# Performance work log

Hardware: AMD Instinct MI355X
Metric: run time of the kernel (lower is better)

The kernel has to match this reference:

```python
import jax, jax.numpy as jnp
import numpy as np

EMBED_DIM = 1024
N_HEADS = 16
DK = EMBED_DIM // N_HEADS


def setup_inputs() -> dict:
    key = jax.random.key(0)
    ks = jax.random.split(key, 9)
    s = 1.0 / np.sqrt(EMBED_DIM)
    d = EMBED_DIM
    return {
        "x": jax.random.normal(ks[0], (2, 2048, d), dtype=jnp.float32),
        "Wq": jax.random.uniform(ks[1], (d, d), jnp.float32, -s, s),
        "bq": jax.random.uniform(ks[2], (d,), jnp.float32, -s, s),
        "Wk": jax.random.uniform(ks[3], (d, d), jnp.float32, -s, s),
        "bk": jax.random.uniform(ks[4], (d,), jnp.float32, -s, s),
        "Wv": jax.random.uniform(ks[5], (d, d), jnp.float32, -s, s),
        "bv": jax.random.uniform(ks[6], (d,), jnp.float32, -s, s),
        "Wo": jax.random.uniform(ks[7], (d, d), jnp.float32, -s, s),
        "bo": jax.random.uniform(ks[8], (d,), jnp.float32, -s, s),
    }


def reference(x, Wq, bq, Wk, bk, Wv, bv, Wo, bo):
    B, S, D = x.shape
    H, dk = N_HEADS, DK
    # QKV projections
    q = (x @ Wq + bq).reshape(B, S, H, dk).transpose(0, 2, 1, 3)  # [B,H,S,dk]
    k = (x @ Wk + bk).reshape(B, S, H, dk).transpose(0, 2, 1, 3)
    v = (x @ Wv + bv).reshape(B, S, H, dk).transpose(0, 2, 1, 3)
    # scaled dot-product attention with full score matrix (faithful to source)
    scores = jnp.einsum("bhqd,bhkd->bhqk", q, k) / jnp.sqrt(jnp.float32(dk))
    attn = jax.nn.softmax(scores, axis=-1)
    out = jnp.einsum("bhqk,bhkd->bhqd", attn, v)  # [B,H,S,dk]
    out = out.transpose(0, 2, 1, 3).reshape(B, S, D)
    return out @ Wo + bo
```

## Files before the change

### kernel.cpp

```cpp
#include <hip/hip_runtime.h>

typedef unsigned short u16;
typedef unsigned int u32;
typedef __attribute__((ext_vector_type(8))) short short8;
typedef __attribute__((ext_vector_type(4))) float float4v;

struct alignas(8) U16x4 { u16 x, y, z, w; };

__device__ __forceinline__ u16 f2b(float f) {
    union { float f; unsigned int u; } v; v.f = f;
    unsigned int r = (v.u >> 16) & 1u;
    v.u += 0x7fffu + r;
    return (u16)(v.u >> 16);
}

__device__ __forceinline__ float b2f(u16 u) {
    union { unsigned int u; float f; } v; v.u = ((u32)u) << 16; return v.f;
}

__device__ __forceinline__ void gld16(const u16* g, u16* l) {
    __builtin_amdgcn_global_load_lds(
        (const __attribute__((address_space(1))) void*)g,
        (__attribute__((address_space(3))) void*)l, 16, 0, 0);
}

__device__ __forceinline__ short8 frag8(const u16* base, int row, int cg) {
    return *(const short8*)(base + row * 64 + ((cg ^ (row & 7)) << 3));
}

__global__ __launch_bounds__(256) void prep_kernel(
    const float* __restrict__ x, const float* __restrict__ W0,
    const float* __restrict__ W1, const float* __restrict__ W2,
    const float* __restrict__ W3, u16* __restrict__ xb,
    u16* __restrict__ T0, u16* __restrict__ T1,
    u16* __restrict__ T2, u16* __restrict__ T3) {
    __shared__ float tile[32][33];
    int id = blockIdx.x;
    if (id < 4096) {
        size_t i = ((size_t)id * 256 + threadIdx.x) * 4;
        float4 v = *(const float4*)(x + i);
        U16x4 o;
        o.x = f2b(v.x); o.y = f2b(v.y); o.z = f2b(v.z); o.w = f2b(v.w);
        *(U16x4*)(xb + i) = o;
        return;
    }
    int r = id - 4096;
    int z = r >> 10, tl = r & 1023;
    const float* W = (z == 0) ? W0 : (z == 1) ? W1 : (z == 2) ? W2 : W3;
    u16* T = (z == 0) ? T0 : (z == 1) ? T1 : (z == 2) ? T2 : T3;
    int t = threadIdx.x;
    int tx = t & 31, ty = t >> 5;
    int bn = (tl & 31) * 32, bk = (tl >> 5) * 32;
#pragma unroll
    for (int p = 0; p < 4; ++p) {
        int k = ty + p * 8;
        tile[k][tx] = W[(size_t)(bk + k) * 1024 + bn + tx];
    }
    __syncthreads();
#pragma unroll
    for (int p = 0; p < 4; ++p) {
        int n = ty + p * 8;
        T[(size_t)(bn + n) * 1024 + bk + tx] = f2b(tile[tx][n]);
    }
}

__global__ __launch_bounds__(512, 2) void qkv_kernel(
    const u16* __restrict__ X,
    const u16* __restrict__ WqT, const u16* __restrict__ WkT, const u16* __restrict__ WvT,
    const float* __restrict__ bq, const float* __restrict__ bk, const float* __restrict__ bv,
    u16* __restrict__ Qo, u16* __restrict__ Ko, u16* __restrict__ VTo) {
    __shared__ __align__(16) u16 As[128 * 64];
    __shared__ __align__(16) u16 Bs[3][128 * 64];
    int id = blockIdx.x;
    int m = (id & 7) | (((id >> 3) & 3) << 3);
    int n = id >> 5;
    int t = threadIdx.x;
    int m0 = m * 128, n0 = n * 128;
    int lane = t & 63, wid = t >> 6;
    int wr = wid >> 2, wc = wid & 3;
    int l16 = lane & 15, quad = lane >> 4;
    int rl = lane >> 3, cs = lane & 7;

    int tileid = wid >> 1, half = wid & 1;
    const u16* gsrc = (tileid == 0) ? X : (tileid == 1) ? WqT
                     : (tileid == 2) ? WkT : WvT;
    int gbase = (tileid == 0) ? m0 : n0;
    u16* ldst = (tileid == 0) ? As : &Bs[tileid - 1][0];

    float4v acc[3][4][2];
    float4v zero4 = {0.f, 0.f, 0.f, 0.f};
#pragma unroll
    for (int z = 0; z < 3; ++z)
#pragma unroll
        for (int i = 0; i < 4; ++i)
#pragma unroll
            for (int j = 0; j < 2; ++j) acc[z][i][j] = zero4;

    for (int k0 = 0; k0 < 1024; k0 += 64) {
        __syncthreads();
#pragma unroll
        for (int p = 0; p < 8; ++p) {
            int q = half * 8 + p;
            int row = q * 8 + rl;
            int c = cs ^ (row & 7);
            gld16(gsrc + (size_t)(gbase + row) * 1024 + k0 + c * 8, ldst + q * 512);
        }
        __syncthreads();
#pragma unroll
        for (int ks = 0; ks < 64; ks += 32) {
            int cg = (ks >> 3) + quad;
            short8 af[4];
#pragma unroll
            for (int i = 0; i < 4; ++i)
                af[i] = frag8(As, wr * 64 + i * 16 + l16, cg);
#pragma unroll
            for (int z = 0; z < 3; ++z) {
                short8 bf[2];
#pragma unroll
                for (int j = 0; j < 2; ++j)
                    bf[j] = frag8(&Bs[z][0], wc * 32 + j * 16 + l16, cg);
#pragma unroll
                for (int i = 0; i < 4; ++i)
#pragma unroll
                    for (int j = 0; j < 2; ++j)
                        acc[z][i][j] = __builtin_amdgcn_mfma_f32_16x16x32_bf16(
                            af[i], bf[j], acc[z][i][j], 0, 0, 0);
            }
        }
    }

    const float QSCALE = 0.18033688011112042f;
#pragma unroll
    for (int j = 0; j < 2; ++j) {
        int n1 = n0 + wc * 32 + j * 16 + l16;
        float bql = bq[n1], bkl = bk[n1], bvl = bv[n1];
#pragma unroll
        for (int i = 0; i < 4; ++i) {
            int mbase = m0 + wr * 64 + i * 16 + quad * 4;
#pragma unroll
            for (int r = 0; r < 4; ++r) {
                Qo[(size_t)(mbase + r) * 1024 + n1] =
                    f2b((acc[0][i][j][r] + bql) * QSCALE);
                Ko[(size_t)(mbase + r) * 1024 + n1] =
                    f2b(acc[1][i][j][r] + bkl);
            }
            int bidx = mbase >> 11, s = mbase & 2047;
            size_t base =
                ((size_t)((bidx * 16 + (n1 >> 6)) * 64 + (n1 & 63))) * 2048 + s;
            U16x4 pk;
            pk.x = f2b(acc[2][i][j][0] + bvl);
            pk.y = f2b(acc[2][i][j][1] + bvl);
            pk.z = f2b(acc[2][i][j][2] + bvl);
            pk.w = f2b(acc[2][i][j][3] + bvl);
            *(U16x4*)(VTo + base) = pk;
        }
    }
}

__global__ __launch_bounds__(256) void oproj_kernel(const u16* __restrict__ X,
                                                    const u16* __restrict__ WoT,
                                                    const float* __restrict__ bias,
                                                    float* __restrict__ out) {
    __shared__ __align__(16) u16 As[64 * 64];
    __shared__ __align__(16) u16 Bs[128 * 64];
    int id = blockIdx.x;
    int m = (id & 7) | (((id >> 3) & 7) << 3);
    int n = id >> 6;
    int t = threadIdx.x;
    int m0 = m * 64, n0 = n * 128;
    int lane = t & 63, wid = t >> 6;
    int l16 = lane & 15, quad = lane >> 4;
    int rl = lane >> 3, cs = lane & 7;

    float4v acc[4][2];
    float4v zero4 = {0.f, 0.f, 0.f, 0.f};
#pragma unroll
    for (int i = 0; i < 4; ++i)
#pragma unroll
        for (int j = 0; j < 2; ++j) acc[i][j] = zero4;

    for (int k0 = 0; k0 < 1024; k0 += 64) {
        __syncthreads();
#pragma unroll
        for (int p = 0; p < 2; ++p) {
            int blk = wid * 2 + p;
            int row = blk * 8 + rl;
            int c = cs ^ (row & 7);
            gld16(X + (size_t)(m0 + row) * 1024 + k0 + c * 8, As + blk * 512);
        }
#pragma unroll
        for (int p = 0; p < 4; ++p) {
            int blk = wid * 4 + p;
            int row = blk * 8 + rl;
            int c = cs ^ (row & 7);
            gld16(WoT + (size_t)(n0 + row) * 1024 + k0 + c * 8, Bs + blk * 512);
        }
        __syncthreads();
#pragma unroll
        for (int ks = 0; ks < 64; ks += 32) {
            int cg = (ks >> 3) + quad;
            short8 af[4], bf[2];
#pragma unroll
            for (int i = 0; i < 4; ++i) af[i] = frag8(As, i * 16 + l16, cg);
#pragma unroll
            for (int j = 0; j < 2; ++j) bf[j] = frag8(Bs, wid * 32 + j * 16 + l16, cg);
#pragma unroll
            for (int i = 0; i < 4; ++i)
#pragma unroll
                for (int j = 0; j < 2; ++j)
                    acc[i][j] = __builtin_amdgcn_mfma_f32_16x16x32_bf16(
                        af[i], bf[j], acc[i][j], 0, 0, 0);
        }
    }

#pragma unroll
    for (int j = 0; j < 2; ++j) {
        int n1 = n0 + wid * 32 + j * 16 + l16;
        float bvl = bias[n1];
#pragma unroll
        for (int i = 0; i < 4; ++i) {
            int mbase = m0 + i * 16 + quad * 4;
#pragma unroll
            for (int r = 0; r < 4; ++r)
                out[(size_t)(mbase + r) * 1024 + n1] = acc[i][j][r] + bvl;
        }
    }
}

__global__ __launch_bounds__(256, 2) void flash_kernel(const u16* __restrict__ Q,
                                                       const u16* __restrict__ Kn,
                                                       const u16* __restrict__ VT,
                                                       u16* __restrict__ Opart,
                                                       float* __restrict__ lpart) {
    __shared__ __align__(16) u16 Ks[2][64 * 64];
    __shared__ __align__(16) u16 Vs[2][64 * 64];
    __shared__ __align__(16) u16 Ps[256 * 64];

    int id = blockIdx.x;
    int bh = (id & 7) | (((id >> 3) & 3) << 3);
    int rest = id >> 5;
    int qb = rest & 7, kvz = rest >> 3;
    int b = bh >> 4, h = bh & 15;
    int t = threadIdx.x;
    int wid = t >> 6, lane = t & 63;
    int l16 = lane & 15, quad = lane >> 4;
    int rl = lane >> 3, cs = lane & 7;
    int q0 = qb * 256 + wid * 64;
    size_t kbase = (size_t)(b * 2048) * 1024 + h * 64;
    size_t vbase = (size_t)(bh * 64) * 2048;
    int kv0 = kvz * 1024;

    short8 qf[4][2];
#pragma unroll
    for (int j = 0; j < 4; ++j)
#pragma unroll
        for (int kk = 0; kk < 2; ++kk)
            qf[j][kk] = *(const short8*)(
                Q + ((size_t)(b * 2048 + q0 + j * 16 + l16)) * 1024 + h * 64 +
                kk * 32 + quad * 8);

    float4v oacc[4][4];
    float lreg[4];
    float4v zero4 = {0.f, 0.f, 0.f, 0.f};
#pragma unroll
    for (int ip = 0; ip < 4; ++ip) {
        lreg[ip] = 0.f;
#pragma unroll
        for (int jd = 0; jd < 4; ++jd) oacc[ip][jd] = zero4;
    }

#define STAGE_KV(buf, kv)                                                     \
    {                                                                         \
        _Pragma("unroll") for (int p2 = 0; p2 < 2; ++p2) {                    \
            int p = wid * 2 + p2;                                             \
            int row = p * 8 + rl;                                             \
            int c = cs ^ (row & 7);                                           \
            gld16(Kn + kbase + (size_t)((kv) + row) * 1024 + c * 8,           \
                  &Ks[buf][p * 512]);                                         \
            gld16(VT + vbase + (size_t)row * 2048 + (kv) + c * 8,             \
                  &Vs[buf][p * 512]);                                         \
        }                                                                     \
    }

    STAGE_KV(0, kv0);

    for (int kvi = 0; kvi < 16; ++kvi) {
        int buf = kvi & 1;
        __syncthreads();
        if (kvi + 1 < 16) STAGE_KV(buf ^ 1, kv0 + (kvi + 1) * 64);

#pragma unroll
        for (int i = 0; i < 4; ++i) {
            float4v sacc[4];
#pragma unroll
            for (int j = 0; j < 4; ++j) sacc[j] = zero4;
            __builtin_amdgcn_s_setprio(1);
#pragma unroll
            for (int kk = 0; kk < 2; ++kk) {
                short8 kf = frag8(&Ks[buf][0], i * 16 + l16, kk * 4 + quad);
#pragma unroll
                for (int j = 0; j < 4; ++j)
                    sacc[j] = __builtin_amdgcn_mfma_f32_16x16x32_bf16(
                        kf, qf[j][kk], sacc[j], 0, 0, 0);
            }
            __builtin_amdgcn_s_setprio(0);
#pragma unroll
            for (int j = 0; j < 4; ++j) {
                float e0f = __builtin_amdgcn_exp2f(sacc[j][0]);
                float e1f = __builtin_amdgcn_exp2f(sacc[j][1]);
                float e2f = __builtin_amdgcn_exp2f(sacc[j][2]);
                float e3f = __builtin_amdgcn_exp2f(sacc[j][3]);
                lreg[j] += (e0f + e1f) + (e2f + e3f);
                u32 e0 = __float_as_uint(e0f) + 0x8000u;
                u32 e1 = __float_as_uint(e1f) + 0x8000u;
                u32 e2 = __float_as_uint(e2f) + 0x8000u;
                u32 e3 = __float_as_uint(e3f) + 0x8000u;
                uint2 pk;
                pk.x = __builtin_amdgcn_perm(e1, e0, 0x07060302u);
                pk.y = __builtin_amdgcn_perm(e3, e2, 0x07060302u);
                int prow = wid * 64 + j * 16 + l16;
                *(uint2*)(Ps + prow * 64 +
                          (((i * 2 + (quad >> 1)) ^ (prow & 7)) << 3) +
                          ((quad & 1) << 2)) = pk;
            }
        }

        __builtin_amdgcn_s_setprio(1);
#pragma unroll
        for (int kk = 0; kk < 2; ++kk) {
            int cg = kk * 4 + quad;
            short8 pf[4];
#pragma unroll
            for (int ip = 0; ip < 4; ++ip)
                pf[ip] = frag8(Ps, wid * 64 + ip * 16 + l16, cg);
#pragma unroll
            for (int jd = 0; jd < 4; ++jd) {
                short8 vf = frag8(&Vs[buf][0], jd * 16 + l16, cg);
#pragma unroll
                for (int ip = 0; ip < 4; ++ip)
                    oacc[ip][jd] = __builtin_amdgcn_mfma_f32_16x16x32_bf16(
                        pf[ip], vf, oacc[ip][jd], 0, 0, 0);
            }
        }
        __builtin_amdgcn_s_setprio(0);
    }
#undef STAGE_KV

#pragma unroll
    for (int j = 0; j < 4; ++j) {
        lreg[j] += __shfl_xor(lreg[j], 16);
        lreg[j] += __shfl_xor(lreg[j], 32);
    }

    size_t obase = (size_t)kvz * 4194304;
#pragma unroll
    for (int ip = 0; ip < 4; ++ip)
#pragma unroll
        for (int r = 0; r < 4; ++r) {
            int q = q0 + ip * 16 + quad * 4 + r;
#pragma unroll
            for (int jd = 0; jd < 4; ++jd)
                Opart[obase + ((size_t)(b * 2048 + q)) * 1024 + h * 64 +
                      jd * 16 + l16] = f2b(oacc[ip][jd][r]);
        }
    if (quad == 0) {
#pragma unroll
        for (int j = 0; j < 4; ++j) {
            int q = q0 + j * 16 + l16;
            lpart[kvz * 65536 + (b * 2048 + q) * 16 + h] = lreg[j];
        }
    }
}

__global__ __launch_bounds__(256) void combine_kernel(const u16* __restrict__ Op,
                                                      const float* __restrict__ lp,
                                                      u16* __restrict__ out) {
    int idx = blockIdx.x * 256 + threadIdx.x;
    size_t i = (size_t)idx * 4;
    int qg = idx >> 8;
    int d = (idx & 255) * 4;
    int h = d >> 6;
    float l0 = lp[qg * 16 + h], l1 = lp[65536 + qg * 16 + h];
    float inv = 1.0f / (l0 + l1);
    U16x4 o0 = *(const U16x4*)(Op + i);
    U16x4 o1 = *(const U16x4*)(Op + 4194304 + i);
    U16x4 o;
    o.x = f2b((b2f(o0.x) + b2f(o1.x)) * inv);
    o.y = f2b((b2f(o0.y) + b2f(o1.y)) * inv);
    o.z = f2b((b2f(o0.z) + b2f(o1.z)) * inv);
    o.w = f2b((b2f(o0.w) + b2f(o1.w)) * inv);
    *(U16x4*)(out + i) = o;
}

extern "C" void kernel_launch(void* const* d_in, const int* in_sizes, int n_in,
                              void* d_out, int out_size, void* d_ws, size_t ws_size,
                              hipStream_t stream) {
    const float* x  = (const float*)d_in[0];
    const float* Wq = (const float*)d_in[1];
    const float* bq = (const float*)d_in[2];
    const float* Wk = (const float*)d_in[3];
    const float* bk = (const float*)d_in[4];
    const float* Wv = (const float*)d_in[5];
    const float* bv = (const float*)d_in[6];
    const float* Wo = (const float*)d_in[7];
    const float* bo = (const float*)d_in[8];
    float* out = (float*)d_out;

    char* ws = (char*)d_ws;
    const size_t MB = 1024 * 1024;
    u16* xb  = (u16*)(ws);
    u16* wqt = (u16*)(ws + 8 * MB);
    u16* wkt = (u16*)(ws + 10 * MB);
    u16* wvt = (u16*)(ws + 12 * MB);
    u16* wot = (u16*)(ws + 14 * MB);
    u16* qb_ = (u16*)(ws + 16 * MB);
    u16* kb_ = (u16*)(ws + 24 * MB);
    u16* vt_ = (u16*)(ws + 32 * MB);
    u16* ab_ = (u16*)(ws + 40 * MB);
    u16* op_ = (u16*)(ws + 48 * MB);
    float* lp_ = (float*)(ws + 64 * MB);

    prep_kernel<<<8192, 256, 0, stream>>>(x, Wq, Wk, Wv, Wo, xb,
                                          wqt, wkt, wvt, wot);
    qkv_kernel<<<256, 512, 0, stream>>>(xb, wqt, wkt, wvt, bq, bk, bv,
                                        qb_, kb_, vt_);
    flash_kernel<<<512, 256, 0, stream>>>(qb_, kb_, vt_, op_, lp_);
    combine_kernel<<<4096, 256, 0, stream>>>(op_, lp_, ab_);
    oproj_kernel<<<512, 256, 0, stream>>>(ab_, wot, bo, out);
}
```

Measured before the change: 193.5 us.

## Keep softmax probabilities in registers via permuted K rows, drop LDS P buffer

The flash kernel no longer writes the exponentiated scores to shared memory and reads them back as MFMA A-operands. Instead, K rows are staged in a permuted order so that each lane's S accumulator fragment already matches the layout needed for the P·V MFMA, and packed bf16 probabilities are fed straight from registers. Dropping the 32KB P buffer and halving the queries per block (128 instead of 256, grid doubled) lowers LDS use and register pressure, allowing 4 blocks per CU. The cost is that K/V tiles are reloaded by twice as many blocks, and each wave does fewer MFMAs per K/V fragment load.

```diff
diff --git a/kernel.cpp b/kernel.cpp
--- a/kernel.cpp
+++ b/kernel.cpp
@@ -4,6 +4,7 @@
 typedef unsigned int u32;
 typedef __attribute__((ext_vector_type(8))) short short8;
 typedef __attribute__((ext_vector_type(4))) float float4v;
+typedef __attribute__((ext_vector_type(4))) unsigned int uint4v;
 
 struct alignas(8) U16x4 { u16 x, y, z, w; };
 
@@ -227,43 +228,42 @@
     }
 }
 
-__global__ __launch_bounds__(256, 2) void flash_kernel(const u16* __restrict__ Q,
+__global__ __launch_bounds__(256, 4) void flash_kernel(const u16* __restrict__ Q,
                                                        const u16* __restrict__ Kn,
                                                        const u16* __restrict__ VT,
                                                        u16* __restrict__ Opart,
                                                        float* __restrict__ lpart) {
     __shared__ __align__(16) u16 Ks[2][64 * 64];
     __shared__ __align__(16) u16 Vs[2][64 * 64];
-    __shared__ __align__(16) u16 Ps[256 * 64];
 
     int id = blockIdx.x;
     int bh = (id & 7) | (((id >> 3) & 3) << 3);
     int rest = id >> 5;
-    int qb = rest & 7, kvz = rest >> 3;
+    int qb = rest & 15, kvz = rest >> 4;
     int b = bh >> 4, h = bh & 15;
     int t = threadIdx.x;
     int wid = t >> 6, lane = t & 63;
     int l16 = lane & 15, quad = lane >> 4;
     int rl = lane >> 3, cs = lane & 7;
-    int q0 = qb * 256 + wid * 64;
+    int q0 = qb * 128 + wid * 32;
     size_t kbase = (size_t)(b * 2048) * 1024 + h * 64;
     size_t vbase = (size_t)(bh * 64) * 2048;
     int kv0 = kvz * 1024;
 
-    short8 qf[4][2];
-#pragma unroll
-    for (int j = 0; j < 4; ++j)
+    short8 qf[2][2];
+#pragma unroll
+    for (int j = 0; j < 2; ++j)
 #pragma unroll
         for (int kk = 0; kk < 2; ++kk)
             qf[j][kk] = *(const short8*)(
                 Q + ((size_t)(b * 2048 + q0 + j * 16 + l16)) * 1024 + h * 64 +
                 kk * 32 + quad * 8);
 
-    float4v oacc[4][4];
-    float lreg[4];
+    float4v oacc[2][4];
+    float lreg[2];
     float4v zero4 = {0.f, 0.f, 0.f, 0.f};
 #pragma unroll
-    for (int ip = 0; ip < 4; ++ip) {
+    for (int ip = 0; ip < 2; ++ip) {
         lreg[ip] = 0.f;
 #pragma unroll
         for (int jd = 0; jd < 4; ++jd) oacc[ip][jd] = zero4;
@@ -275,7 +275,9 @@
             int p = wid * 2 + p2;                                             \
             int row = p * 8 + rl;                                             \
             int c = cs ^ (row & 7);                                           \
-            gld16(Kn + kbase + (size_t)((kv) + row) * 1024 + c * 8,           \
+            int key = (((row >> 4) & 1) << 5) | (((row >> 2) & 3) << 3) |     \
+                      (((row >> 5) & 1) << 2) | (row & 3);                    \
+            gld16(Kn + kbase + (size_t)((kv) + key) * 1024 + c * 8,           \
                   &Ks[buf][p * 512]);                                         \
             gld16(VT + vbase + (size_t)row * 2048 + (kv) + c * 8,             \
                   &Vs[buf][p * 512]);                                         \
@@ -289,39 +291,32 @@
         __syncthreads();
         if (kvi + 1 < 16) STAGE_KV(buf ^ 1, kv0 + (kvi + 1) * 64);
 
+        u32 pw[2][4][2];
 #pragma unroll
         for (int i = 0; i < 4; ++i) {
-            float4v sacc[4];
-#pragma unroll
-            for (int j = 0; j < 4; ++j) sacc[j] = zero4;
+            float4v s0 = zero4, s1 = zero4;
             __builtin_amdgcn_s_setprio(1);
 #pragma unroll
             for (int kk = 0; kk < 2; ++kk) {
                 short8 kf = frag8(&Ks[buf][0], i * 16 + l16, kk * 4 + quad);
-#pragma unroll
-                for (int j = 0; j < 4; ++j)
-                    sacc[j] = __builtin_amdgcn_mfma_f32_16x16x32_bf16(
-                        kf, qf[j][kk], sacc[j], 0, 0, 0);
+                s0 = __builtin_amdgcn_mfma_f32_16x16x32_bf16(kf, qf[0][kk], s0, 0, 0, 0);
+                s1 = __builtin_amdgcn_mfma_f32_16x16x32_bf16(kf, qf[1][kk], s1, 0, 0, 0);
             }
             __builtin_amdgcn_s_setprio(0);
 #pragma unroll
-            for (int j = 0; j < 4; ++j) {
-                float e0f = __builtin_amdgcn_exp2f(sacc[j][0]);
-                float e1f = __builtin_amdgcn_exp2f(sacc[j][1]);
-                float e2f = __builtin_amdgcn_exp2f(sacc[j][2]);
-                float e3f = __builtin_amdgcn_exp2f(sacc[j][3]);
+            for (int j = 0; j < 2; ++j) {
+                float4v s = (j == 0) ? s0 : s1;
+                float e0f = __builtin_amdgcn_exp2f(s[0]);
+                float e1f = __builtin_amdgcn_exp2f(s[1]);
+                float e2f = __builtin_amdgcn_exp2f(s[2]);
+                float e3f = __builtin_amdgcn_exp2f(s[3]);
                 lreg[j] += (e0f + e1f) + (e2f + e3f);
                 u32 e0 = __float_as_uint(e0f) + 0x8000u;
                 u32 e1 = __float_as_uint(e1f) + 0x8000u;
                 u32 e2 = __float_as_uint(e2f) + 0x8000u;
                 u32 e3 = __float_as_uint(e3f) + 0x8000u;
-                uint2 pk;
-                pk.x = __builtin_amdgcn_perm(e1, e0, 0x07060302u);
-                pk.y = __builtin_amdgcn_perm(e3, e2, 0x07060302u);
-                int prow = wid * 64 + j * 16 + l16;
-                *(uint2*)(Ps + prow * 64 +
-                          (((i * 2 + (quad >> 1)) ^ (prow & 7)) << 3) +
-                          ((quad & 1) << 2)) = pk;
+                pw[j][i][0] = __builtin_amdgcn_perm(e1, e0, 0x07060302u);
+                pw[j][i][1] = __builtin_amdgcn_perm(e3, e2, 0x07060302u);
             }
         }
 
@@ -329,17 +324,19 @@
 #pragma unroll
         for (int kk = 0; kk < 2; ++kk) {
             int cg = kk * 4 + quad;
-            short8 pf[4];
-#pragma unroll
-            for (int ip = 0; ip < 4; ++ip)
-                pf[ip] = frag8(Ps, wid * 64 + ip * 16 + l16, cg);
-#pragma unroll
-            for (int jd = 0; jd < 4; ++jd) {
-                short8 vf = frag8(&Vs[buf][0], jd * 16 + l16, cg);
-#pragma unroll
-                for (int ip = 0; ip < 4; ++ip)
-                    oacc[ip][jd] = __builtin_amdgcn_mfma_f32_16x16x32_bf16(
-                        pf[ip], vf, oacc[ip][jd], 0, 0, 0);
+            short8 vf[4];
+#pragma unroll
+            for (int jd = 0; jd < 4; ++jd)
+                vf[jd] = frag8(&Vs[buf][0], jd * 16 + l16, cg);
+#pragma unroll
+            for (int j = 0; j < 2; ++j) {
+                union { uint4v u; short8 s; } pu;
+                pu.u = (uint4v){pw[j][kk][0], pw[j][kk][1],
+                                pw[j][2 + kk][0], pw[j][2 + kk][1]};
+#pragma unroll
+                for (int jd = 0; jd < 4; ++jd)
+                    oacc[j][jd] = __builtin_amdgcn_mfma_f32_16x16x32_bf16(
+                        pu.s, vf[jd], oacc[j][jd], 0, 0, 0);
             }
         }
         __builtin_amdgcn_s_setprio(0);
@@ -347,14 +344,14 @@
 #undef STAGE_KV
 
 #pragma unroll
-    for (int j = 0; j < 4; ++j) {
+    for (int j = 0; j < 2; ++j) {
         lreg[j] += __shfl_xor(lreg[j], 16);
         lreg[j] += __shfl_xor(lreg[j], 32);
     }
 
     size_t obase = (size_t)kvz * 4194304;
 #pragma unroll
-    for (int ip = 0; ip < 4; ++ip)
+    for (int ip = 0; ip < 2; ++ip)
 #pragma unroll
         for (int r = 0; r < 4; ++r) {
             int q = q0 + ip * 16 + quad * 4 + r;
@@ -365,7 +362,7 @@
         }
     if (quad == 0) {
 #pragma unroll
-        for (int j = 0; j < 4; ++j) {
+        for (int j = 0; j < 2; ++j) {
             int q = q0 + j * 16 + l16;
             lpart[kvz * 65536 + (b * 2048 + q) * 16 + h] = lreg[j];
         }
@@ -424,7 +421,7 @@
                                           wqt, wkt, wvt, wot);
     qkv_kernel<<<256, 512, 0, stream>>>(xb, wqt, wkt, wvt, bq, bk, bv,
                                         qb_, kb_, vt_);
-    flash_kernel<<<512, 256, 0, stream>>>(qb_, kb_, vt_, op_, lp_);
+    flash_kernel<<<1024, 256, 0, stream>>>(qb_, kb_, vt_, op_, lp_);
     combine_kernel<<<4096, 256, 0, stream>>>(op_, lp_, ab_);
     oproj_kernel<<<512, 256, 0, stream>>>(ab_, wot, bo, out);
 }
```

New measurement: 189.4 us. -2.1%, faster.
